# Performance work log

Measured on AMD Instinct MI355X. Metric: run time of the kernel, lower is better.

The kernel has to match this reference:

```python
import jax, jax.numpy as jnp
import numpy as np

B, S, D_MODEL, D_FF = 8, 1024, 512, 2048
NCAT, NSUB, TOPK = 8, 8, 2
E = NCAT * NSUB            # 64 experts
CAP = 1024


def setup_inputs() -> dict:
    key = jax.random.key(0)
    ks = jax.random.split(key, 6)
    hidden = jax.random.normal(ks[0], (B, S, D_MODEL), jnp.float32)
    cat_indices = jax.random.randint(ks[1], (B, S, TOPK), 0, NCAT)
    sub_indices = jax.random.randint(ks[2], (B, S, TOPK), 0, NSUB)
    weights = jax.random.uniform(ks[3], (B, S, TOPK), jnp.float32)
    # Stacked per-expert MLP params (Expert = Linear -> GELU -> Linear, dropout off in eval)
    W1 = jax.random.normal(ks[4], (E, D_MODEL, D_FF), jnp.float32) / np.sqrt(D_MODEL).astype(np.float32)
    b1 = jnp.zeros((E, D_FF), jnp.float32)
    W2 = jax.random.normal(ks[5], (E, D_FF, D_MODEL), jnp.float32) / np.sqrt(D_FF).astype(np.float32)
    b2 = jnp.zeros((E, D_MODEL), jnp.float32)
    return dict(hidden=hidden, cat_indices=cat_indices, sub_indices=sub_indices,
                weights=weights, W1=W1, b1=b1, W2=W2, b2=b2)


def _moe_forward(hidden, cat_indices, sub_indices, weights, W1, b1, W2, b2):
    Bq, Sq, d = hidden.shape
    K = cat_indices.shape[-1]
    T = Bq * Sq            # tokens
    A = T * K              # (token, k) routing assignments
    x = hidden.reshape(T, d)
    eid = (cat_indices * NSUB + sub_indices).reshape(A).astype(jnp.int32)  # flat expert id
    wf = weights.reshape(A)
    tok = jnp.arange(A, dtype=jnp.int32) // K  # token index per assignment

    # position of each assignment within its expert's capacity buffer
    oh = jax.nn.one_hot(eid, E, dtype=jnp.int32)                     # [A, E]
    pos = jnp.take_along_axis(jnp.cumsum(oh, axis=0) - 1,
                              eid[:, None].astype(jnp.int32), axis=1)[:, 0]
    valid = (pos < CAP).astype(hidden.dtype)

    # dispatch: gather tokens into [E, CAP, d] buffer (overflow dropped; CAP sized to avoid it)
    buf = jnp.zeros((E, CAP, d), hidden.dtype).at[eid, pos].set(x[tok], mode='drop')

    # grouped expert MLP: Linear -> GELU -> Linear
    h = jax.nn.gelu(jnp.einsum('ecd,edf->ecf', buf, W1) + b1[:, None, :], approximate=False)
    yb = jnp.einsum('ecf,efd->ecd', h, W2) + b2[:, None, :]          # [E, CAP, d]

    # combine: gather each assignment's expert output, weight it, scatter-add over tokens
    pc = jnp.minimum(pos, CAP - 1)
    ya = yb[eid, pc] * (wf * valid)[:, None]                          # [A, d]
    out = jnp.zeros((T, d), hidden.dtype).at[tok].add(ya)
    return out.reshape(Bq, Sq, d)


def reference(hidden, cat_indices, sub_indices, weights, W1, b1, W2, b2):
    return _moe_forward(hidden, cat_indices, sub_indices, weights, W1, b1, W2, b2)
```

## Files before the change

kernel.cpp:

```cpp
#include <hip/hip_runtime.h>
#include <hip/hip_bf16.h>
#include <cstdint>
#include <cstddef>

#define TOKENS 8192
#define ASSIGN 16384
#define DM     512
#define DFF    2048
#define NEXP   64
#define NSUB_  8
#define CAP2   512
#define BK     64
#define BMT    256

typedef __bf16 bf16;
typedef __bf16 bf16x4 __attribute__((ext_vector_type(4)));
typedef __bf16 bf16x8 __attribute__((ext_vector_type(8)));
typedef float  f32x4  __attribute__((ext_vector_type(4)));

__global__ void k_zero(int* __restrict__ count) { count[threadIdx.x] = 0; }

__global__ void k_route(const int* __restrict__ cat, const int* __restrict__ sub,
                        int* __restrict__ count, int* __restrict__ slot_of) {
    int a = blockIdx.x * 256 + threadIdx.x;
    if (a >= ASSIGN) return;
    int e = cat[a] * NSUB_ + sub[a];
    int s = atomicAdd(&count[e], 1);
    slot_of[a] = (s < CAP2) ? (e * CAP2 + s) : -1;
}

__global__ void k_gather(const float* __restrict__ hidden, const int* __restrict__ slot_of,
                         bf16* __restrict__ xg) {
    int a = blockIdx.x * 4 + (threadIdx.x >> 6);
    int t = threadIdx.x & 63;
    int r = slot_of[a];
    if (r < 0) return;
    int tok = a >> 1;
    const f32x4* src = (const f32x4*)(hidden + (size_t)tok * DM);
    f32x4 v0 = src[t * 2], v1 = src[t * 2 + 1];
    bf16x8 o;
    o[0] = (bf16)v0[0]; o[1] = (bf16)v0[1]; o[2] = (bf16)v0[2]; o[3] = (bf16)v0[3];
    o[4] = (bf16)v1[0]; o[5] = (bf16)v1[1]; o[6] = (bf16)v1[2]; o[7] = (bf16)v1[3];
    *(bf16x8*)(xg + (size_t)r * DM + t * 8) = o;
}

__device__ inline void gload_lds16(const void* g, void* l) {
    __builtin_amdgcn_global_load_lds((const __attribute__((address_space(1))) void*)g,
                                     (__attribute__((address_space(3))) void*)l, 16, 0, 0);
}

template <bool GELU>
__global__ __launch_bounds__(512, 4)
void k_gemm(const bf16* __restrict__ A, const float* __restrict__ W,
            const float* __restrict__ bias, bf16* __restrict__ C,
            const int* __restrict__ count, int N, int K, int ntn) {
    __shared__ __align__(16) char As[BMT * 128];
    __shared__ __align__(16) char Bs[128 * 128];

    int nwg = gridDim.x;
    int lg = (int)(blockIdx.x & 7) * (nwg >> 3) + (int)(blockIdx.x >> 3);
    int e = lg / (2 * ntn);
    int rem = lg - e * 2 * ntn;
    int ntile = rem >> 1, mtile = rem & 1;

    int mc = count[e]; if (mc > CAP2) mc = CAP2;
    if (mtile * BMT >= mc) return;
    int tid = threadIdx.x, wave = tid >> 6, lane = tid & 63;
    int wm = wave >> 1, wn = wave & 1;

    const char*  Ag = (const char*)(A + (size_t)(e * CAP2 + mtile * BMT) * K);
    const float* Wg = W + (size_t)e * K * N + (size_t)ntile * 128;

    int kq = ((lane >> 3) & 7) | ((wave & 1) << 3);
    int nq = (lane & 7) | (((wave >> 1) & 3) << 3);

    f32x4 br[4];
    auto issueB = [&](int kt) {
        const float* p = Wg + (size_t)(kt * BK + kq * 4) * N + nq * 4;
        br[0] = *(const f32x4*)(p);
        br[1] = *(const f32x4*)(p + N);
        br[2] = *(const f32x4*)(p + 2 * (size_t)N);
        br[3] = *(const f32x4*)(p + 3 * (size_t)N);
    };
    auto writeB = [&]() {
#pragma unroll
        for (int c = 0; c < 4; c++) {
            int n = nq * 4 + c;
            bf16x4 v;
#pragma unroll
            for (int j = 0; j < 4; j++) v[j] = (bf16)br[j][c];
            *(bf16x4*)(Bs + n * 128 + ((kq * 8) ^ ((n & 7) << 4))) = v;
        }
    };
    auto issueA = [&](int kt) {
#pragma unroll
        for (int i = 0; i < 4; i++) {
            int chunk = i * 8 + wave;
            int d = chunk * 1024 + lane * 16;
            int row = d >> 7;
            int col = (d & 127) ^ ((row & 7) << 4);
            gload_lds16(Ag + (size_t)row * (2 * K) + (size_t)kt * 128 + col,
                        As + chunk * 1024);
        }
    };

    f32x4 acc[4][4];
#pragma unroll
    for (int i = 0; i < 4; i++)
#pragma unroll
        for (int j = 0; j < 4; j++) acc[i][j] = f32x4{0.f, 0.f, 0.f, 0.f};

    issueB(0);
    int nK = K >> 6;
    for (int kt = 0; kt < nK; kt++) {
        issueA(kt);
        asm volatile("s_waitcnt vmcnt(0)" ::: "memory");
        writeB();
        if (kt + 1 < nK) issueB(kt + 1);
        asm volatile("s_waitcnt lgkmcnt(0)" ::: "memory");
        __builtin_amdgcn_s_barrier();
        __builtin_amdgcn_sched_barrier(0);
#pragma unroll
        for (int ks = 0; ks < 2; ks++) {
            bf16x8 af[4], bfv[4];
#pragma unroll
            for (int mi = 0; mi < 4; mi++) {
                int row = wm * 64 + mi * 16 + (lane & 15);
                af[mi] = *(const bf16x8*)(As + row * 128 +
                         ((ks * 64 + (lane >> 4) * 16) ^ ((row & 7) << 4)));
            }
#pragma unroll
            for (int ni = 0; ni < 4; ni++) {
                int n = wn * 64 + ni * 16 + (lane & 15);
                bfv[ni] = *(const bf16x8*)(Bs + n * 128 +
                          ((ks * 64 + (lane >> 4) * 16) ^ ((n & 7) << 4)));
            }
#pragma unroll
            for (int mi = 0; mi < 4; mi++)
#pragma unroll
                for (int ni = 0; ni < 4; ni++)
                    acc[mi][ni] = __builtin_amdgcn_mfma_f32_16x16x32_bf16(
                        af[mi], bfv[ni], acc[mi][ni], 0, 0, 0);
        }
        __builtin_amdgcn_sched_barrier(0);
        __builtin_amdgcn_s_barrier();
    }

#pragma unroll
    for (int mi = 0; mi < 4; mi++) {
        int rowb = wm * 64 + mi * 16 + ((lane >> 4) << 2);
#pragma unroll
        for (int ni = 0; ni < 4; ni++) {
            int col = ntile * 128 + wn * 64 + ni * 16 + (lane & 15);
            float bv = bias[e * N + col];
#pragma unroll
            for (int r = 0; r < 4; r++) {
                float v = acc[mi][ni][r] + bv;
                if (GELU) v = 0.5f * v * (1.0f + erff(v * 0.70710678118654752f));
                int grow = e * CAP2 + mtile * BMT + rowb + r;
                C[(size_t)grow * N + col] = (bf16)v;
            }
        }
    }
}

__global__ void k_combine(const float* __restrict__ wts, const int* __restrict__ slot_of,
                          const bf16* __restrict__ y, float* __restrict__ out) {
    int tok = blockIdx.x * 4 + (threadIdx.x >> 6);
    int t = threadIdx.x & 63;
    float acc[8] = {0, 0, 0, 0, 0, 0, 0, 0};
#pragma unroll
    for (int k = 0; k < 2; k++) {
        int a = tok * 2 + k;
        int r = slot_of[a];
        if (r >= 0) {
            float w = wts[a];
            bf16x8 v = *(const bf16x8*)(y + (size_t)r * DM + t * 8);
#pragma unroll
            for (int j = 0; j < 8; j++) acc[j] += w * (float)v[j];
        }
    }
    f32x4* o = (f32x4*)(out + (size_t)tok * DM + t * 8);
    o[0] = f32x4{acc[0], acc[1], acc[2], acc[3]};
    o[1] = f32x4{acc[4], acc[5], acc[6], acc[7]};
}

extern "C" void kernel_launch(void* const* d_in, const int* in_sizes, int n_in,
                              void* d_out, int out_size, void* d_ws, size_t ws_size,
                              hipStream_t stream) {
    const float* hidden = (const float*)d_in[0];
    const int*   cat    = (const int*)d_in[1];
    const int*   sub    = (const int*)d_in[2];
    const float* wts    = (const float*)d_in[3];
    const float* W1     = (const float*)d_in[4];
    const float* b1     = (const float*)d_in[5];
    const float* W2     = (const float*)d_in[6];
    const float* b2     = (const float*)d_in[7];
    float* out = (float*)d_out;

    char* ws = (char*)d_ws;
    size_t off = 0;
    bf16* hbuf = (bf16*)(ws + off); off += (size_t)NEXP * CAP2 * DFF * 2;
    bf16* xg   = (bf16*)(ws + off); off += (size_t)NEXP * CAP2 * DM * 2;
    bf16* y    = xg;
    int* count   = (int*)(ws + off); off += 256;
    int* slot_of = (int*)(ws + off); off += (size_t)ASSIGN * 4;

    k_zero<<<1, 64, 0, stream>>>(count);
    k_route<<<ASSIGN / 256, 256, 0, stream>>>(cat, sub, count, slot_of);
    k_gather<<<ASSIGN / 4, 256, 0, stream>>>(hidden, slot_of, xg);

    k_gemm<true><<<dim3(NEXP * 16 * 2), 512, 0, stream>>>(
        xg, W1, b1, hbuf, count, DFF, DM, 16);

    k_gemm<false><<<dim3(NEXP * 4 * 2), 512, 0, stream>>>(
        hbuf, W2, b2, y, count, DM, DFF, 4);

    k_combine<<<TOKENS / 4, 256, 0, stream>>>(wts, slot_of, y, out);
}
```

Before: 307.5 us.

## Double-buffer A tile in LDS and switch GELU to tanh approximation

Adds a second LDS buffer for the A tile so the global-to-LDS load for the next k-step is issued before the MFMA work on the current one, moving the vmcnt wait to the end of the iteration. The aim is to overlap A and B global loads with compute instead of stalling at the top of each step. It also replaces the erf-based GELU with a tanh approximation built from a sigmoid and exp, which makes the epilogue cheaper but departs slightly from the exact GELU the reference uses. The doubled LDS use may lower occupancy.

Result: slower. 314.9 us (+2.4%).

```diff
diff --git a/kernel.cpp b/kernel.cpp
--- a/kernel.cpp
+++ b/kernel.cpp
@@ -44,6 +44,13 @@
     *(bf16x8*)(xg + (size_t)r * DM + t * 8) = o;
 }
 
+__device__ inline float gelu_tanh(float x) {
+    float s2 = 1.5957691216057308f * x * (1.0f + 0.044715f * x * x);
+    float z = __expf(-fabsf(s2));
+    float sig = 1.0f / (1.0f + z);
+    return (s2 >= 0.0f) ? x * sig : x * (1.0f - sig);
+}
+
 __device__ inline void gload_lds16(const void* g, void* l) {
     __builtin_amdgcn_global_load_lds((const __attribute__((address_space(1))) void*)g,
                                      (__attribute__((address_space(3))) void*)l, 16, 0, 0);
@@ -54,7 +61,7 @@
 void k_gemm(const bf16* __restrict__ A, const float* __restrict__ W,
             const float* __restrict__ bias, bf16* __restrict__ C,
             const int* __restrict__ count, int N, int K, int ntn) {
-    __shared__ __align__(16) char As[BMT * 128];
+    __shared__ __align__(16) char As[2][BMT * 128];
     __shared__ __align__(16) char Bs[128 * 128];
 
     int nwg = gridDim.x;
@@ -92,7 +99,7 @@
             *(bf16x4*)(Bs + n * 128 + ((kq * 8) ^ ((n & 7) << 4))) = v;
         }
     };
-    auto issueA = [&](int kt) {
+    auto issueA = [&](int kt, char* dst) {
 #pragma unroll
         for (int i = 0; i < 4; i++) {
             int chunk = i * 8 + wave;
@@ -100,7 +107,7 @@
             int row = d >> 7;
             int col = (d & 127) ^ ((row & 7) << 4);
             gload_lds16(Ag + (size_t)row * (2 * K) + (size_t)kt * 128 + col,
-                        As + chunk * 1024);
+                        dst + chunk * 1024);
         }
     };
 
@@ -110,13 +117,19 @@
 #pragma unroll
         for (int j = 0; j < 4; j++) acc[i][j] = f32x4{0.f, 0.f, 0.f, 0.f};
 
+    int nK = K >> 6;
     issueB(0);
-    int nK = K >> 6;
+    issueA(0, As[0]);
+    asm volatile("s_waitcnt vmcnt(0)" ::: "memory");
+    __builtin_amdgcn_sched_barrier(0);
+
     for (int kt = 0; kt < nK; kt++) {
-        issueA(kt);
-        asm volatile("s_waitcnt vmcnt(0)" ::: "memory");
+        int c = kt & 1, n = c ^ 1;
         writeB();
-        if (kt + 1 < nK) issueB(kt + 1);
+        if (kt + 1 < nK) {
+            issueB(kt + 1);
+            issueA(kt + 1, As[n]);
+        }
         asm volatile("s_waitcnt lgkmcnt(0)" ::: "memory");
         __builtin_amdgcn_s_barrier();
         __builtin_amdgcn_sched_barrier(0);
@@ -126,14 +139,14 @@
 #pragma unroll
             for (int mi = 0; mi < 4; mi++) {
                 int row = wm * 64 + mi * 16 + (lane & 15);
-                af[mi] = *(const bf16x8*)(As + row * 128 +
+                af[mi] = *(const bf16x8*)(As[c] + row * 128 +
                          ((ks * 64 + (lane >> 4) * 16) ^ ((row & 7) << 4)));
             }
 #pragma unroll
             for (int ni = 0; ni < 4; ni++) {
-                int n = wn * 64 + ni * 16 + (lane & 15);
-                bfv[ni] = *(const bf16x8*)(Bs + n * 128 +
-                          ((ks * 64 + (lane >> 4) * 16) ^ ((n & 7) << 4)));
+                int nn = wn * 64 + ni * 16 + (lane & 15);
+                bfv[ni] = *(const bf16x8*)(Bs + nn * 128 +
+                          ((ks * 64 + (lane >> 4) * 16) ^ ((nn & 7) << 4)));
             }
 #pragma unroll
             for (int mi = 0; mi < 4; mi++)
@@ -143,7 +156,9 @@
                         af[mi], bfv[ni], acc[mi][ni], 0, 0, 0);
         }
         __builtin_amdgcn_sched_barrier(0);
+        asm volatile("s_waitcnt vmcnt(0)" ::: "memory");
         __builtin_amdgcn_s_barrier();
+        __builtin_amdgcn_sched_barrier(0);
     }
 
 #pragma unroll
@@ -156,7 +171,7 @@
 #pragma unroll
             for (int r = 0; r < 4; r++) {
                 float v = acc[mi][ni][r] + bv;
-                if (GELU) v = 0.5f * v * (1.0f + erff(v * 0.70710678118654752f));
+                if (GELU) v = gelu_tanh(v);
                 int grow = e * CAP2 + mtile * BMT + rowb + r;
                 C[(size_t)grow * N + col] = (bf16)v;
             }
```
